# Kernel tuning notes

Measured on AMD Instinct MI355X. Metric: run time of the kernel, lower is better.

The kernel has to match this reference:

```python
import jax, jax.numpy as jnp
import numpy as np

ALPHA = 2.0   # snntorch ATan surrogate default
THRESH = 1.0  # snntorch Leaky default threshold

@jax.custom_vjp
def spike(x):
    return (x > 0).astype(x.dtype)

def _spike_fwd(x):
    return spike(x), x

def _spike_bwd(x, g):
    # ATan surrogate gradient: (alpha/2) / (1 + (pi/2 * alpha * x)^2)
    return (g * (ALPHA / 2) / (1 + (jnp.pi / 2 * ALPHA * x) ** 2),)

spike.defvjp(_spike_fwd, _spike_bwd)

def _lif(inp, mem, beta):
    # snntorch Leaky, reset_mechanism='subtract':
    # reset from previous mem (detached), then integrate, then fire
    reset = jax.lax.stop_gradient(spike(mem - THRESH))
    mem = jnp.clip(beta, 0.0, 1.0) * mem + inp - reset * THRESH
    spk = spike(mem - THRESH)
    return spk, mem

def setup_inputs() -> dict:
    key = jax.random.key(0)
    ks = jax.random.split(key, 8)
    V, H, T, B = 32000, 512, 512, 8
    s = 0.02
    inv = 1.0 / np.sqrt(H)
    return {
        "x": jax.random.randint(ks[0], (T, B), 0, V),
        "emb": jax.random.normal(ks[1], (V, H), jnp.float32) * s,
        "pos_emb": jax.random.normal(ks[2], (T, H), jnp.float32) * s,
        "beta1": jnp.full((H,), 0.9, jnp.float32),
        "beta2": jnp.full((H,), 0.9, jnp.float32),
        "beta3": jnp.full((H,), 0.9, jnp.float32),
        "W2": jax.random.normal(ks[3], (H, H), jnp.float32) * inv,
        "b2": jnp.zeros((H,), jnp.float32),
        "W3": jax.random.normal(ks[4], (H, H), jnp.float32) * inv,
        "b3": jnp.zeros((H,), jnp.float32),
        "Wout": jax.random.normal(ks[5], (V, H), jnp.float32) * inv,
        "bout": jnp.zeros((V,), jnp.float32),
    }

def reference(x, emb, pos_emb, beta1, beta2, beta3, W2, b2, W3, b3, Wout, bout):
    T, B = x.shape
    H = emb.shape[1]
    # precompute token + positional embedding for all steps: [T, B, H]
    hid = emb[x] + pos_emb[:, None, :]
    mem0 = jnp.zeros((B, H), emb.dtype)

    def step(carry, h_t):
        m1, m2, m3 = carry
        spk1, m1 = _lif(h_t, m1, beta1)
        h = jax.nn.relu(spk1 @ W2.T + b2)
        spk2, m2 = _lif(h, m2, beta2)
        h = jax.nn.relu(spk2 @ W3.T + b3)
        spk3, m3 = _lif(h, m3, beta3)
        logits = spk3 @ Wout.T + bout  # [B, V]
        return (m1, m2, m3), logits

    _, out = jax.lax.scan(step, (mem0, mem0, mem0), hid)
    return out  # [T, B, V]
```

## Files before the change

kernel.cpp:

```cpp
#include <hip/hip_runtime.h>

#define TT 512
#define BB 8
#define HH 512
#define VV 32000
#define RR (TT * BB)

__device__ __forceinline__ float clip01(float x) { return fminf(fmaxf(x, 0.0f), 1.0f); }

__global__ void gather_kernel(const int* __restrict__ x, const float* __restrict__ emb,
                              const float* __restrict__ pos, float* __restrict__ hid,
                              int* __restrict__ cnt_all) {
    int r = blockIdx.x;
    int h = threadIdx.x;
    int t = r >> 3;
    int xv = x[r];
    hid[((size_t)r << 9) + h] = emb[((size_t)xv << 9) + h] + pos[(t << 9) + h];
    if (r < 3 * RR / HH)
        cnt_all[(r << 9) + h] = 0;
}

__global__ void lif1_kernel(const float* __restrict__ hid, const float* __restrict__ beta,
                            int* __restrict__ cnt, int* __restrict__ act) {
    int b = blockIdx.x;
    int h = threadIdx.x;
    const float* base = hid + ((size_t)b << 9) + h;
    float bt = clip01(beta[h]);
    float m = 0.0f;
    for (int t0 = 0; t0 < TT; t0 += 16) {
        float inp[16];
#pragma unroll
        for (int u = 0; u < 16; ++u) inp[u] = base[(size_t)(t0 + u) * (BB * HH)];
#pragma unroll
        for (int u = 0; u < 16; ++u) {
            float reset = (m > 1.0f) ? 1.0f : 0.0f;
            m = bt * m + inp[u] - reset;
            if (m > 1.0f) {
                int r = (t0 + u) * BB + b;
                int p = atomicAdd(&cnt[r], 1);
                act[(r << 9) + p] = h;
            }
        }
    }
}

__global__ void lif_fused_kernel(const int* __restrict__ cnt_in, const int* __restrict__ act_in,
                                 const float* __restrict__ W, const float* __restrict__ bias,
                                 const float* __restrict__ beta,
                                 int* __restrict__ cnt_out, int* __restrict__ act_out) {
    __shared__ int c[TT];
    int b = blockIdx.x;
    int h = threadIdx.x;
    c[h] = cnt_in[h * BB + b];
    __syncthreads();
    float bh = bias[h];
    float inp0 = fmaxf(bh, 0.0f);
    float bt = clip01(beta[h]);
    float m = 0.0f;
    for (int t0 = 0; t0 < TT; t0 += 16) {
        int n[16];
#pragma unroll
        for (int u = 0; u < 16; ++u) n[u] = c[t0 + u];
#pragma unroll
        for (int u = 0; u < 16; ++u) {
            float inp;
            if (n[u] == 0) {
                inp = inp0;
            } else {
                float acc = bh;
                const int* a = act_in + (((t0 + u) * BB + b) << 9);
                for (int i = 0; i < n[u]; ++i) acc += W[(h << 9) + a[i]];
                inp = fmaxf(acc, 0.0f);
            }
            float reset = (m > 1.0f) ? 1.0f : 0.0f;
            m = bt * m + inp - reset;
            if (m > 1.0f) {
                int r = (t0 + u) * BB + b;
                int p = atomicAdd(&cnt_out[r], 1);
                act_out[(r << 9) + p] = h;
            }
        }
    }
}

__global__ void out_gemm_kernel(const int* __restrict__ cnt, const int* __restrict__ act,
                                const float* __restrict__ Wout, const float* __restrict__ bout,
                                float* __restrict__ out) {
    int v = blockIdx.x * 2048 + threadIdx.x * 4;
    if (v >= VV) return;
    float4 bv = *(const float4*)(bout + v);
    int r0 = blockIdx.y * 8;
#pragma unroll
    for (int rr = 0; rr < 8; ++rr) {
        int r = r0 + rr;
        int n = cnt[r];
        float4 acc = bv;
        const int* a = act + (r << 9);
        for (int i = 0; i < n; ++i) {
            int k = a[i];
            acc.x += Wout[(size_t)(v + 0) * HH + k];
            acc.y += Wout[(size_t)(v + 1) * HH + k];
            acc.z += Wout[(size_t)(v + 2) * HH + k];
            acc.w += Wout[(size_t)(v + 3) * HH + k];
        }
        *(float4*)(out + (size_t)r * VV + v) = acc;
    }
}

extern "C" void kernel_launch(void* const* d_in, const int* in_sizes, int n_in,
                              void* d_out, int out_size, void* d_ws, size_t ws_size,
                              hipStream_t stream) {
    const int*   x     = (const int*)d_in[0];
    const float* emb   = (const float*)d_in[1];
    const float* pos   = (const float*)d_in[2];
    const float* beta1 = (const float*)d_in[3];
    const float* beta2 = (const float*)d_in[4];
    const float* beta3 = (const float*)d_in[5];
    const float* W2    = (const float*)d_in[6];
    const float* b2    = (const float*)d_in[7];
    const float* W3    = (const float*)d_in[8];
    const float* b3    = (const float*)d_in[9];
    const float* Wout  = (const float*)d_in[10];
    const float* bout  = (const float*)d_in[11];
    float* out = (float*)d_out;

    float* hid  = (float*)d_ws;
    int*   act1 = (int*)(hid + (size_t)RR * HH);
    int*   act2 = act1 + (size_t)RR * HH;
    int*   act3 = act2 + (size_t)RR * HH;
    int*   cnt1 = act3 + (size_t)RR * HH;
    int*   cnt2 = cnt1 + RR;
    int*   cnt3 = cnt2 + RR;

    gather_kernel<<<RR, HH, 0, stream>>>(x, emb, pos, hid, cnt1);
    lif1_kernel<<<BB, HH, 0, stream>>>(hid, beta1, cnt1, act1);
    lif_fused_kernel<<<BB, HH, 0, stream>>>(cnt1, act1, W2, b2, beta2, cnt2, act2);
    lif_fused_kernel<<<BB, HH, 0, stream>>>(cnt2, act2, W3, b3, beta3, cnt3, act3);
    out_gemm_kernel<<<dim3(16, RR / 8), HH, 0, stream>>>(cnt3, act3, Wout, bout, out);
}
```

Measured before the change: 681.9 us.

## Fuse gather and three LIF layers into one scan kernel with LDS counters

Merges the embedding gather, layer-1 LIF and the two sparse LIF layers into a single kernel per batch element. Spike counters live in shared memory instead of global atomics, and the hid intermediate buffer is dropped because embeddings are read directly inside the layer-1 loop. The output GEMM now writes with nontemporal stores. This removes three launches, a global round trip and global atomics. In exchange the per-timestep work runs on only 8 blocks, and the gather moves onto that serialized path.

```diff
diff --git a/kernel.cpp b/kernel.cpp
--- a/kernel.cpp
+++ b/kernel.cpp
@@ -6,86 +6,124 @@
 #define VV 32000
 #define RR (TT * BB)
 
+typedef float v4f __attribute__((ext_vector_type(4)));
+
 __device__ __forceinline__ float clip01(float x) { return fminf(fmaxf(x, 0.0f), 1.0f); }
 
-__global__ void gather_kernel(const int* __restrict__ x, const float* __restrict__ emb,
-                              const float* __restrict__ pos, float* __restrict__ hid,
-                              int* __restrict__ cnt_all) {
-    int r = blockIdx.x;
-    int h = threadIdx.x;
-    int t = r >> 3;
-    int xv = x[r];
-    hid[((size_t)r << 9) + h] = emb[((size_t)xv << 9) + h] + pos[(t << 9) + h];
-    if (r < 3 * RR / HH)
-        cnt_all[(r << 9) + h] = 0;
-}
+__global__ void __launch_bounds__(512) snn_scan_kernel(
+        const int* __restrict__ x, const float* __restrict__ emb,
+        const float* __restrict__ pos,
+        const float* __restrict__ beta1, const float* __restrict__ beta2,
+        const float* __restrict__ beta3,
+        const float* __restrict__ W2, const float* __restrict__ b2,
+        const float* __restrict__ W3, const float* __restrict__ b3,
+        int* __restrict__ act1, int* __restrict__ act2, int* __restrict__ act3,
+        int* __restrict__ cnt3_g) {
+    __shared__ int x_lds[TT];
+    __shared__ int c1[TT], c2[TT], c3[TT];
+    const int b = blockIdx.x;
+    const int h = threadIdx.x;
 
-__global__ void lif1_kernel(const float* __restrict__ hid, const float* __restrict__ beta,
-                            int* __restrict__ cnt, int* __restrict__ act) {
-    int b = blockIdx.x;
-    int h = threadIdx.x;
-    const float* base = hid + ((size_t)b << 9) + h;
-    float bt = clip01(beta[h]);
-    float m = 0.0f;
-    for (int t0 = 0; t0 < TT; t0 += 16) {
-        float inp[16];
+    x_lds[h] = x[h * BB + b];
+    c1[h] = 0; c2[h] = 0; c3[h] = 0;
+    __syncthreads();
+
+    {
+        float bt = clip01(beta1[h]);
+        float m = 0.0f;
+        for (int t0 = 0; t0 < TT; t0 += 32) {
+            float ev[32], pv[32];
 #pragma unroll
-        for (int u = 0; u < 16; ++u) inp[u] = base[(size_t)(t0 + u) * (BB * HH)];
+            for (int u = 0; u < 32; ++u) {
+                int xv = x_lds[t0 + u];
+                ev[u] = emb[((size_t)xv << 9) + h];
+                pv[u] = pos[((t0 + u) << 9) + h];
+            }
 #pragma unroll
-        for (int u = 0; u < 16; ++u) {
-            float reset = (m > 1.0f) ? 1.0f : 0.0f;
-            m = bt * m + inp[u] - reset;
-            if (m > 1.0f) {
-                int r = (t0 + u) * BB + b;
-                int p = atomicAdd(&cnt[r], 1);
-                act[(r << 9) + p] = h;
+            for (int u = 0; u < 32; ++u) {
+                float inp = ev[u] + pv[u];
+                float reset = (m > 1.0f) ? 1.0f : 0.0f;
+                m = bt * m + inp - reset;
+                if (m > 1.0f) {
+                    int t = t0 + u;
+                    int p = atomicAdd(&c1[t], 1);
+                    act1[((t * BB + b) << 9) + p] = h;
+                }
             }
         }
     }
-}
+    __syncthreads();
 
-__global__ void lif_fused_kernel(const int* __restrict__ cnt_in, const int* __restrict__ act_in,
-                                 const float* __restrict__ W, const float* __restrict__ bias,
-                                 const float* __restrict__ beta,
-                                 int* __restrict__ cnt_out, int* __restrict__ act_out) {
-    __shared__ int c[TT];
-    int b = blockIdx.x;
-    int h = threadIdx.x;
-    c[h] = cnt_in[h * BB + b];
-    __syncthreads();
-    float bh = bias[h];
-    float inp0 = fmaxf(bh, 0.0f);
-    float bt = clip01(beta[h]);
-    float m = 0.0f;
-    for (int t0 = 0; t0 < TT; t0 += 16) {
-        int n[16];
+    {
+        float bh = b2[h];
+        float inp0 = fmaxf(bh, 0.0f);
+        float bt = clip01(beta2[h]);
+        float m = 0.0f;
+        for (int t0 = 0; t0 < TT; t0 += 16) {
+            int n[16];
 #pragma unroll
-        for (int u = 0; u < 16; ++u) n[u] = c[t0 + u];
+            for (int u = 0; u < 16; ++u) n[u] = c1[t0 + u];
 #pragma unroll
-        for (int u = 0; u < 16; ++u) {
-            float inp;
-            if (n[u] == 0) {
-                inp = inp0;
-            } else {
-                float acc = bh;
-                const int* a = act_in + (((t0 + u) * BB + b) << 9);
-                for (int i = 0; i < n[u]; ++i) acc += W[(h << 9) + a[i]];
-                inp = fmaxf(acc, 0.0f);
-            }
-            float reset = (m > 1.0f) ? 1.0f : 0.0f;
-            m = bt * m + inp - reset;
-            if (m > 1.0f) {
-                int r = (t0 + u) * BB + b;
-                int p = atomicAdd(&cnt_out[r], 1);
-                act_out[(r << 9) + p] = h;
+            for (int u = 0; u < 16; ++u) {
+                float inp;
+                if (n[u] == 0) {
+                    inp = inp0;
+                } else {
+                    float acc = bh;
+                    const int* a = act1 + (((t0 + u) * BB + b) << 9);
+                    for (int i = 0; i < n[u]; ++i) acc += W2[(h << 9) + a[i]];
+                    inp = fmaxf(acc, 0.0f);
+                }
+                float reset = (m > 1.0f) ? 1.0f : 0.0f;
+                m = bt * m + inp - reset;
+                if (m > 1.0f) {
+                    int t = t0 + u;
+                    int p = atomicAdd(&c2[t], 1);
+                    act2[((t * BB + b) << 9) + p] = h;
+                }
             }
         }
     }
+    __syncthreads();
+
+    {
+        float bh = b3[h];
+        float inp0 = fmaxf(bh, 0.0f);
+        float bt = clip01(beta3[h]);
+        float m = 0.0f;
+        for (int t0 = 0; t0 < TT; t0 += 16) {
+            int n[16];
+#pragma unroll
+            for (int u = 0; u < 16; ++u) n[u] = c2[t0 + u];
+#pragma unroll
+            for (int u = 0; u < 16; ++u) {
+                float inp;
+                if (n[u] == 0) {
+                    inp = inp0;
+                } else {
+                    float acc = bh;
+                    const int* a = act2 + (((t0 + u) * BB + b) << 9);
+                    for (int i = 0; i < n[u]; ++i) acc += W3[(h << 9) + a[i]];
+                    inp = fmaxf(acc, 0.0f);
+                }
+                float reset = (m > 1.0f) ? 1.0f : 0.0f;
+                m = bt * m + inp - reset;
+                if (m > 1.0f) {
+                    int t = t0 + u;
+                    int p = atomicAdd(&c3[t], 1);
+                    act3[((t * BB + b) << 9) + p] = h;
+                }
+            }
+        }
+    }
+    __syncthreads();
+    cnt3_g[h * BB + b] = c3[h];
 }
 
-__global__ void out_gemm_kernel(const int* __restrict__ cnt, const int* __restrict__ act,
-                                const float* __restrict__ Wout, const float* __restrict__ bout,
-                                float* __restrict__ out) {
+__global__ void __launch_bounds__(512) out_gemm_kernel(
+        const int* __restrict__ cnt, const int* __restrict__ act,
+        const float* __restrict__ Wout, const float* __restrict__ bout,
+        float* __restrict__ out) {
     int v = blockIdx.x * 2048 + threadIdx.x * 4;
     if (v >= VV) return;
     float4 bv = *(const float4*)(bout + v);
@@ -103,7 +141,8 @@
             acc.z += Wout[(size_t)(v + 2) * HH + k];
             acc.w += Wout[(size_t)(v + 3) * HH + k];
         }
-        *(float4*)(out + (size_t)r * VV + v) = acc;
+        v4f st = {acc.x, acc.y, acc.z, acc.w};
+        __builtin_nontemporal_store(st, (v4f*)(out + (size_t)r * VV + v));
     }
 }
 
@@ -124,17 +163,12 @@
     const float* bout  = (const float*)d_in[11];
     float* out = (float*)d_out;
 
-    float* hid  = (float*)d_ws;
-    int*   act1 = (int*)(hid + (size_t)RR * HH);
-    int*   act2 = act1 + (size_t)RR * HH;
-    int*   act3 = act2 + (size_t)RR * HH;
-    int*   cnt1 = act3 + (size_t)RR * HH;
-    int*   cnt2 = cnt1 + RR;
-    int*   cnt3 = cnt2 + RR;
+    int* act1 = (int*)d_ws;
+    int* act2 = act1 + (size_t)RR * HH;
+    int* act3 = act2 + (size_t)RR * HH;
+    int* cnt3 = act3 + (size_t)RR * HH;
 
-    gather_kernel<<<RR, HH, 0, stream>>>(x, emb, pos, hid, cnt1);
-    lif1_kernel<<<BB, HH, 0, stream>>>(hid, beta1, cnt1, act1);
-    lif_fused_kernel<<<BB, HH, 0, stream>>>(cnt1, act1, W2, b2, beta2, cnt2, act2);
-    lif_fused_kernel<<<BB, HH, 0, stream>>>(cnt2, act2, W3, b3, beta3, cnt3, act3);
+    snn_scan_kernel<<<BB, HH, 0, stream>>>(x, emb, pos, beta1, beta2, beta3,
+                                           W2, b2, W3, b3, act1, act2, act3, cnt3);
     out_gemm_kernel<<<dim3(16, RR / 8), HH, 0, stream>>>(cnt3, act3, Wout, bout, out);
 }
```

New measurement: 677.5 us. Within noise of the previous version (-0.6%).
